# Kernel optimization log

Hardware: AMD Instinct MI355X
Metric: run time of the kernel (lower is better)

## Reference

```python
import jax, jax.numpy as jnp
import numpy as np

VOCAB, EMBED, HIDDEN = 256, 16, 256
BATCH, SEQ = 128, 512


def setup_inputs() -> dict:
    key = jax.random.key(0)
    ks = jax.random.split(key, 8)
    s = lambda fan_in: 1.0 / np.sqrt(fan_in)
    return {
        "x": jax.random.randint(ks[0], (BATCH, SEQ), 0, VOCAB, dtype=jnp.int32),
        "embed": jax.random.normal(ks[1], (VOCAB, EMBED), dtype=jnp.float32),
        "W_ih": jax.random.uniform(ks[2], (EMBED, 3 * HIDDEN), jnp.float32, -s(EMBED), s(EMBED)),
        "b_ih": jax.random.uniform(ks[3], (3 * HIDDEN,), jnp.float32, -s(EMBED), s(EMBED)),
        "W_hh": jax.random.uniform(ks[4], (HIDDEN, 3 * HIDDEN), jnp.float32, -s(HIDDEN), s(HIDDEN)),
        "b_hh": jax.random.uniform(ks[5], (3 * HIDDEN,), jnp.float32, -s(HIDDEN), s(HIDDEN)),
        "W_out": jax.random.uniform(ks[6], (HIDDEN, VOCAB), jnp.float32, -s(HIDDEN), s(HIDDEN)),
        "b_out": jax.random.uniform(ks[7], (VOCAB,), jnp.float32, -s(HIDDEN), s(HIDDEN)),
    }


def reference(x, embed, W_ih, b_ih, W_hh, b_hh, W_out, b_out):
    B = x.shape[0]
    H = W_hh.shape[0]
    emb = embed[x]                                   # [B, S, E]
    # input-side gate pre-activations can be batched across time (same math)
    gi = jnp.einsum("bse,eg->bsg", emb, W_ih) + b_ih  # [B, S, 3H]

    def step(h, gi_t):
        gh = h @ W_hh + b_hh                          # [B, 3H]
        r_i, z_i, n_i = jnp.split(gi_t, 3, axis=-1)
        r_h, z_h, n_h = jnp.split(gh, 3, axis=-1)
        r = jax.nn.sigmoid(r_i + r_h)
        z = jax.nn.sigmoid(z_i + z_h)
        n = jnp.tanh(n_i + r * n_h)
        h_new = (1.0 - z) * n + z * h
        return h_new, h_new

    h0 = jnp.zeros((B, H), dtype=emb.dtype)
    _, hs = jax.lax.scan(step, h0, jnp.swapaxes(gi, 0, 1))  # hs: [S, B, H]
    h_seq = jnp.swapaxes(hs, 0, 1)                           # [B, S, H]
    return jnp.einsum("bsh,hv->bsv", h_seq, W_out) + b_out   # [B, S, V]
```

## Files before the change

### kernel.cpp

```cpp
#include <hip/hip_runtime.h>
#include <hip/hip_fp16.h>

#define BB 128
#define SS 512
#define EE 16
#define HH 256
#define G3 768
#define VV 256

typedef _Float16 half8 __attribute__((ext_vector_type(8)));
typedef _Float16 half4_t __attribute__((ext_vector_type(4)));
typedef float f32x4 __attribute__((ext_vector_type(4)));

__global__ __launch_bounds__(256) void swizzle_weights(
    const float* __restrict__ Whh, const float* __restrict__ Wout,
    _Float16* __restrict__ whh_swz, _Float16* __restrict__ wout_swz) {
  int t = blockIdx.x * 256 + threadIdx.x;
  if (t < 48 * 8 * 64 * 8) {
    int j = t & 7, L = (t >> 3) & 63, k = (t >> 9) & 7, n = t >> 12;
    int row = k * 32 + (L >> 4) * 8 + j;
    int col = n * 16 + (L & 15);
    whh_swz[t] = (_Float16)Whh[row * G3 + col];
  }
  if (t < 16 * 8 * 64 * 8) {
    int j = t & 7, L = (t >> 3) & 63, k = (t >> 9) & 7, n = t >> 12;
    int row = k * 32 + (L >> 4) * 8 + j;
    int col = n * 16 + (L & 15);
    wout_swz[t] = (_Float16)Wout[row * VV + col];
  }
}

__global__ __launch_bounds__(256) void gi_kernel(
    const int* __restrict__ x, const float* __restrict__ embed,
    const float* __restrict__ W_ih, const float* __restrict__ b_ih,
    const float* __restrict__ b_hh, _Float16* __restrict__ gi_swz) {
  int gid = blockIdx.x;
  int bg = gid >> 7;
  int t0 = (gid & 127) * 4;
  int tid = threadIdx.x;

  __shared__ __align__(16) float s_wih[EE * G3];
  __shared__ __align__(16) float s_bias[G3];
  __shared__ __align__(16) float s_emb16[4][16][EE];
  __shared__ int s_x[4][16];

  for (int i = tid; i < EE * G3; i += 256) s_wih[i] = W_ih[i];
  for (int i = tid; i < G3; i += 256)
    s_bias[i] = b_ih[i] + (i < 512 ? b_hh[i] : 0.0f);
  if (tid < 64) {
    int tt = tid >> 4, m = tid & 15;
    s_x[tt][m] = x[(bg * 16 + m) * SS + t0 + tt];
  }
  __syncthreads();
  for (int i = tid; i < 4 * 16 * EE; i += 256) {
    int tt = i >> 8, m = (i >> 4) & 15, e = i & 15;
    s_emb16[tt][m][e] = embed[s_x[tt][m] * EE + e];
  }
  __syncthreads();

  for (int cch = 0; cch < 3; cch++) {
    int gc = cch * 256 + tid;
    float w[EE];
#pragma unroll
    for (int e = 0; e < EE; e++) w[e] = s_wih[e * G3 + gc];
    float bias = s_bias[gc];
    int wi = (gc >> 4) & 15, cc = gc & 15;
    int tilebase = (cch * 16 + wi) * 64;
    for (int tt = 0; tt < 4; tt++) {
      size_t gbase = (size_t)(bg * 512 + t0 + tt) * 12288;
#pragma unroll
      for (int mq = 0; mq < 4; mq++) {
        half4_t v;
#pragma unroll
        for (int r = 0; r < 4; r++) {
          int m = mq * 4 + r;
          float acc = bias;
#pragma unroll
          for (int e = 0; e < EE; e++) acc += s_emb16[tt][m][e] * w[e];
          v[r] = (_Float16)acc;
        }
        *(half4_t*)(gi_swz + gbase + (size_t)((tilebase + mq * 16 + cc) * 4)) = v;
      }
    }
  }
}

__global__ void __launch_bounds__(1024)
__attribute__((amdgpu_waves_per_eu(4, 4)))
gru_kernel(
    const _Float16* __restrict__ gi_swz, const _Float16* __restrict__ whh_swz,
    const float* __restrict__ b_hh, _Float16* __restrict__ h_seq) {
  int bg = blockIdx.x;
  int tid = threadIdx.x;
  int w = tid >> 6, L = tid & 63;
  int q = L >> 4, c = L & 15;

  __shared__ __align__(16) _Float16 s_h[2][16][264];

  half8 wR[8], wZ[8], wN[8];
#pragma unroll
  for (int k = 0; k < 8; k++) {
    wR[k] = *(const half8*)(whh_swz + (((size_t)((0 * 16 + w) * 8 + k) * 64 + L) * 8));
    wZ[k] = *(const half8*)(whh_swz + (((size_t)((1 * 16 + w) * 8 + k) * 64 + L) * 8));
    wN[k] = *(const half8*)(whh_swz + (((size_t)((2 * 16 + w) * 8 + k) * 64 + L) * 8));
  }
  float bhn = b_hh[512 + w * 16 + c];

  for (int idx = tid; idx < (2 * 16 * 264) / 2; idx += 1024)
    ((unsigned int*)s_h)[idx] = 0u;
  __syncthreads();

  int col = w * 16 + c;
  unsigned hoff = (unsigned)(bg * 16 + q * 4) * (SS * HH) + (unsigned)col;
  unsigned gioff = (unsigned)(bg * 512) * 12288u + (unsigned)((w * 64 + L) * 4);

  int cur = 0;
#pragma unroll 1
  for (int t = 0; t < SS; t++) {
    half4_t giR = *(const half4_t*)(gi_swz + gioff);
    half4_t giZ = *(const half4_t*)(gi_swz + gioff + 4096u);
    half4_t giN = *(const half4_t*)(gi_swz + gioff + 8192u);

    const _Float16* hsrc = &s_h[cur][0][0];
    half4_t hp;
#pragma unroll
    for (int r = 0; r < 4; r++) hp[r] = hsrc[(q * 4 + r) * 264 + col];

    f32x4 aR = {0.f, 0.f, 0.f, 0.f}, aZ = aR, aN = aR;
#pragma unroll
    for (int k = 0; k < 8; k++) {
      half8 av = *(const half8*)(hsrc + c * 264 + k * 32 + q * 8);
      aR = __builtin_amdgcn_mfma_f32_16x16x32_f16(av, wR[k], aR, 0, 0, 0);
      aZ = __builtin_amdgcn_mfma_f32_16x16x32_f16(av, wZ[k], aZ, 0, 0, 0);
      aN = __builtin_amdgcn_mfma_f32_16x16x32_f16(av, wN[k], aN, 0, 0, 0);
    }

    _Float16* hdst = &s_h[cur ^ 1][0][0];
#pragma unroll
    for (int r = 0; r < 4; r++) {
      int m = q * 4 + r;
      float rg = aR[r] + (float)giR[r];
      rg = 1.f / (1.f + __expf(-rg));
      float zg = aZ[r] + (float)giZ[r];
      zg = 1.f / (1.f + __expf(-zg));
      float ng = (float)giN[r] + rg * (aN[r] + bhn);
      ng = 2.f / (1.f + __expf(-2.f * ng)) - 1.f;
      float hn = (1.f - zg) * ng + zg * (float)hp[r];
      hdst[m * 264 + col] = (_Float16)hn;
      h_seq[(size_t)hoff + (unsigned)r * (SS * HH)] = (_Float16)hn;
    }
    __syncthreads();
    cur ^= 1;
    hoff += HH;
    gioff += 12288u;
  }
}

__global__ __launch_bounds__(256) void out_kernel(
    const _Float16* __restrict__ h_seq, const _Float16* __restrict__ wout_swz,
    const float* __restrict__ b_out, float* __restrict__ out) {
  int blk = blockIdx.x;
  int tid = threadIdx.x;
  int w = tid >> 6, L = tid & 63, q = L >> 4, c = L & 15;

  __shared__ __align__(16) _Float16 s_a[64 * 264];

  const _Float16* src = h_seq + (size_t)blk * 64 * 256;
  for (int idx = tid; idx < (64 * 256) / 8; idx += 256) {
    int row = idx >> 5, kk = (idx & 31) * 8;
    *(half8*)(s_a + row * 264 + kk) = *(const half8*)(src + row * 256 + kk);
  }
  __syncthreads();

  half8 a[8];
#pragma unroll
  for (int k = 0; k < 8; k++)
    a[k] = *(const half8*)(s_a + (w * 16 + c) * 264 + k * 32 + q * 8);

  f32x4 acc[16];
#pragma unroll
  for (int n = 0; n < 16; n++) {
    f32x4 z = {0.f, 0.f, 0.f, 0.f};
    acc[n] = z;
#pragma unroll
    for (int k = 0; k < 8; k++) {
      half8 b = *(const half8*)(wout_swz + ((size_t)(n * 8 + k) * 64 + L) * 8);
      acc[n] = __builtin_amdgcn_mfma_f32_16x16x32_f16(a[k], b, acc[n], 0, 0, 0);
    }
  }
#pragma unroll
  for (int n = 0; n < 16; n++) {
    int v = n * 16 + c;
    float bo = b_out[v];
#pragma unroll
    for (int r = 0; r < 4; r++) {
      int bt = blk * 64 + w * 16 + q * 4 + r;
      out[(size_t)bt * 256 + v] = acc[n][r] + bo;
    }
  }
}

extern "C" void kernel_launch(void* const* d_in, const int* in_sizes, int n_in,
                              void* d_out, int out_size, void* d_ws, size_t ws_size,
                              hipStream_t stream) {
  const int*   x    = (const int*)d_in[0];
  const float* emb  = (const float*)d_in[1];
  const float* Wih  = (const float*)d_in[2];
  const float* bih  = (const float*)d_in[3];
  const float* Whh  = (const float*)d_in[4];
  const float* bhh  = (const float*)d_in[5];
  const float* Wout = (const float*)d_in[6];
  const float* bout = (const float*)d_in[7];

  char* ws = (char*)d_ws;
  _Float16* gi_swz   = (_Float16*)(ws);
  _Float16* whh_swz  = (_Float16*)(ws + 100663296);
  _Float16* wout_swz = (_Float16*)(ws + 100663296 + 393216);
  _Float16* h_seq    = (_Float16*)(ws + 100663296 + 393216 + 131072);

  swizzle_weights<<<768, 256, 0, stream>>>(Whh, Wout, whh_swz, wout_swz);
  gi_kernel<<<1024, 256, 0, stream>>>(x, emb, Wih, bih, bhh, gi_swz);
  gru_kernel<<<8, 1024, 0, stream>>>(gi_swz, whh_swz, bhh, h_seq);
  out_kernel<<<1024, 256, 0, stream>>>(h_seq, wout_swz, bout, (float*)d_out);
}
```

Measured before the change: 1.574 ms.

## Halve GRU block waves, each wave computing two column tiles per gate

The recurrent GRU kernel now runs 8 waves per block instead of 16, with each wave owning 32 hidden columns (two 16-wide MFMA tiles per gate). Each h fragment read from shared memory feeds six MFMAs, and fewer waves join the per-timestep barrier. In exchange each wave holds twice as many weight registers and does twice the serial MFMA and gate work per step, which can lengthen the critical path of the latency-bound recurrence.

```diff
diff --git a/kernel.cpp b/kernel.cpp
--- a/kernel.cpp
+++ b/kernel.cpp
@@ -85,8 +85,8 @@
   }
 }
 
-__global__ void __launch_bounds__(1024)
-__attribute__((amdgpu_waves_per_eu(4, 4)))
+__global__ void __launch_bounds__(512)
+__attribute__((amdgpu_waves_per_eu(2, 2)))
 gru_kernel(
     const _Float16* __restrict__ gi_swz, const _Float16* __restrict__ whh_swz,
     const float* __restrict__ b_hh, _Float16* __restrict__ h_seq) {
@@ -97,57 +97,83 @@
 
   __shared__ __align__(16) _Float16 s_h[2][16][264];
 
-  half8 wR[8], wZ[8], wN[8];
-#pragma unroll
-  for (int k = 0; k < 8; k++) {
-    wR[k] = *(const half8*)(whh_swz + (((size_t)((0 * 16 + w) * 8 + k) * 64 + L) * 8));
-    wZ[k] = *(const half8*)(whh_swz + (((size_t)((1 * 16 + w) * 8 + k) * 64 + L) * 8));
-    wN[k] = *(const half8*)(whh_swz + (((size_t)((2 * 16 + w) * 8 + k) * 64 + L) * 8));
-  }
-  float bhn = b_hh[512 + w * 16 + c];
-
-  for (int idx = tid; idx < (2 * 16 * 264) / 2; idx += 1024)
+  half8 wf[3][2][8];
+#pragma unroll
+  for (int g = 0; g < 3; g++)
+#pragma unroll
+    for (int i = 0; i < 2; i++) {
+      int np = g * 16 + 2 * w + i;
+#pragma unroll
+      for (int k = 0; k < 8; k++)
+        wf[g][i][k] = *(const half8*)(whh_swz + (((size_t)(np * 8 + k) * 64 + L) * 8));
+    }
+  float bhn0 = b_hh[512 + w * 32 + c];
+  float bhn1 = b_hh[512 + w * 32 + 16 + c];
+
+  for (int idx = tid; idx < (2 * 16 * 264) / 2; idx += 512)
     ((unsigned int*)s_h)[idx] = 0u;
   __syncthreads();
 
-  int col = w * 16 + c;
-  unsigned hoff = (unsigned)(bg * 16 + q * 4) * (SS * HH) + (unsigned)col;
-  unsigned gioff = (unsigned)(bg * 512) * 12288u + (unsigned)((w * 64 + L) * 4);
+  int col0 = w * 32 + c;
+  unsigned hoff = (unsigned)(bg * 16 + q * 4) * (SS * HH) + (unsigned)col0;
+  unsigned gioff = (unsigned)(bg * 512) * 12288u + (unsigned)(w * 512 + L * 4);
 
   int cur = 0;
 #pragma unroll 1
   for (int t = 0; t < SS; t++) {
-    half4_t giR = *(const half4_t*)(gi_swz + gioff);
-    half4_t giZ = *(const half4_t*)(gi_swz + gioff + 4096u);
-    half4_t giN = *(const half4_t*)(gi_swz + gioff + 8192u);
+    half4_t giR0 = *(const half4_t*)(gi_swz + gioff);
+    half4_t giR1 = *(const half4_t*)(gi_swz + gioff + 256u);
+    half4_t giZ0 = *(const half4_t*)(gi_swz + gioff + 4096u);
+    half4_t giZ1 = *(const half4_t*)(gi_swz + gioff + 4352u);
+    half4_t giN0 = *(const half4_t*)(gi_swz + gioff + 8192u);
+    half4_t giN1 = *(const half4_t*)(gi_swz + gioff + 8448u);
 
     const _Float16* hsrc = &s_h[cur][0][0];
-    half4_t hp;
-#pragma unroll
-    for (int r = 0; r < 4; r++) hp[r] = hsrc[(q * 4 + r) * 264 + col];
-
-    f32x4 aR = {0.f, 0.f, 0.f, 0.f}, aZ = aR, aN = aR;
+    half4_t hp0, hp1;
+#pragma unroll
+    for (int r = 0; r < 4; r++) {
+      hp0[r] = hsrc[(q * 4 + r) * 264 + col0];
+      hp1[r] = hsrc[(q * 4 + r) * 264 + col0 + 16];
+    }
+
+    f32x4 aR0 = {0.f, 0.f, 0.f, 0.f}, aR1 = aR0, aZ0 = aR0, aZ1 = aR0, aN0 = aR0, aN1 = aR0;
 #pragma unroll
     for (int k = 0; k < 8; k++) {
       half8 av = *(const half8*)(hsrc + c * 264 + k * 32 + q * 8);
-      aR = __builtin_amdgcn_mfma_f32_16x16x32_f16(av, wR[k], aR, 0, 0, 0);
-      aZ = __builtin_amdgcn_mfma_f32_16x16x32_f16(av, wZ[k], aZ, 0, 0, 0);
-      aN = __builtin_amdgcn_mfma_f32_16x16x32_f16(av, wN[k], aN, 0, 0, 0);
+      aR0 = __builtin_amdgcn_mfma_f32_16x16x32_f16(av, wf[0][0][k], aR0, 0, 0, 0);
+      aR1 = __builtin_amdgcn_mfma_f32_16x16x32_f16(av, wf[0][1][k], aR1, 0, 0, 0);
+      aZ0 = __builtin_amdgcn_mfma_f32_16x16x32_f16(av, wf[1][0][k], aZ0, 0, 0, 0);
+      aZ1 = __builtin_amdgcn_mfma_f32_16x16x32_f16(av, wf[1][1][k], aZ1, 0, 0, 0);
+      aN0 = __builtin_amdgcn_mfma_f32_16x16x32_f16(av, wf[2][0][k], aN0, 0, 0, 0);
+      aN1 = __builtin_amdgcn_mfma_f32_16x16x32_f16(av, wf[2][1][k], aN1, 0, 0, 0);
     }
 
     _Float16* hdst = &s_h[cur ^ 1][0][0];
 #pragma unroll
     for (int r = 0; r < 4; r++) {
       int m = q * 4 + r;
-      float rg = aR[r] + (float)giR[r];
-      rg = 1.f / (1.f + __expf(-rg));
-      float zg = aZ[r] + (float)giZ[r];
-      zg = 1.f / (1.f + __expf(-zg));
-      float ng = (float)giN[r] + rg * (aN[r] + bhn);
-      ng = 2.f / (1.f + __expf(-2.f * ng)) - 1.f;
-      float hn = (1.f - zg) * ng + zg * (float)hp[r];
-      hdst[m * 264 + col] = (_Float16)hn;
-      h_seq[(size_t)hoff + (unsigned)r * (SS * HH)] = (_Float16)hn;
+      {
+        float rg = aR0[r] + (float)giR0[r];
+        rg = 1.f / (1.f + __expf(-rg));
+        float zg = aZ0[r] + (float)giZ0[r];
+        zg = 1.f / (1.f + __expf(-zg));
+        float ng = (float)giN0[r] + rg * (aN0[r] + bhn0);
+        ng = 2.f / (1.f + __expf(-2.f * ng)) - 1.f;
+        float hn = (1.f - zg) * ng + zg * (float)hp0[r];
+        hdst[m * 264 + col0] = (_Float16)hn;
+        h_seq[(size_t)hoff + (unsigned)r * (SS * HH)] = (_Float16)hn;
+      }
+      {
+        float rg = aR1[r] + (float)giR1[r];
+        rg = 1.f / (1.f + __expf(-rg));
+        float zg = aZ1[r] + (float)giZ1[r];
+        zg = 1.f / (1.f + __expf(-zg));
+        float ng = (float)giN1[r] + rg * (aN1[r] + bhn1);
+        ng = 2.f / (1.f + __expf(-2.f * ng)) - 1.f;
+        float hn = (1.f - zg) * ng + zg * (float)hp1[r];
+        hdst[m * 264 + col0 + 16] = (_Float16)hn;
+        h_seq[(size_t)hoff + (unsigned)r * (SS * HH) + 16u] = (_Float16)hn;
+      }
     }
     __syncthreads();
     cur ^= 1;
@@ -220,6 +246,6 @@
 
   swizzle_weights<<<768, 256, 0, stream>>>(Whh, Wout, whh_swz, wout_swz);
   gi_kernel<<<1024, 256, 0, stream>>>(x, emb, Wih, bih, bhh, gi_swz);
-  gru_kernel<<<8, 1024, 0, stream>>>(gi_swz, whh_swz, bhh, h_seq);
+  gru_kernel<<<8, 512, 0, stream>>>(gi_swz, whh_swz, bhh, h_seq);
   out_kernel<<<1024, 256, 0, stream>>>(h_seq, wout_swz, bout, (float*)d_out);
 }
```

Measured after the change: 1.915 ms. 21.7% more time.
